# Kernel optimization log

Measured on AMD Instinct MI355X. Metric: run time of the kernel, lower is better.

Reference implementation:

```python
import jax, jax.numpy as jnp
import numpy as np

N_HEADS = 8
D_EMBED = 1024
D_CROSS = 768
D_HEAD = D_EMBED // N_HEADS


def setup_inputs() -> dict:
    key = jax.random.key(0)
    ks = jax.random.split(key, 10)
    B, SQ, SKV = 8, 4096, 77
    scale_e = 1.0 / np.sqrt(D_EMBED)
    scale_c = 1.0 / np.sqrt(D_CROSS)
    return {
        "x": jax.random.normal(ks[0], (B, SQ, D_EMBED), dtype=jnp.float32),
        "y": jax.random.normal(ks[1], (B, SKV, D_CROSS), dtype=jnp.float32),
        # weights stored as [in, out] so projection is x @ W + b
        "Wq": jax.random.normal(ks[2], (D_EMBED, D_EMBED), dtype=jnp.float32) * scale_e,
        "bq": jnp.zeros((D_EMBED,), dtype=jnp.float32),
        "Wk": jax.random.normal(ks[3], (D_CROSS, D_EMBED), dtype=jnp.float32) * scale_c,
        "bk": jnp.zeros((D_EMBED,), dtype=jnp.float32),
        "Wv": jax.random.normal(ks[4], (D_CROSS, D_EMBED), dtype=jnp.float32) * scale_c,
        "bv": jnp.zeros((D_EMBED,), dtype=jnp.float32),
        "Wo": jax.random.normal(ks[5], (D_EMBED, D_EMBED), dtype=jnp.float32) * scale_e,
        "bo": jnp.zeros((D_EMBED,), dtype=jnp.float32),
    }


def reference(x, y, Wq, bq, Wk, bk, Wv, bv, Wo, bo):
    B, SQ, _ = x.shape
    # projections
    q = x @ Wq + bq                      # [B, SQ, D_EMBED]
    k = y @ Wk + bk                      # [B, SKV, D_EMBED]
    v = y @ Wv + bv                      # [B, SKV, D_EMBED]
    # split heads -> [B, H, S, Dh]
    q = q.reshape(B, SQ, N_HEADS, D_HEAD).transpose(0, 2, 1, 3)
    k = k.reshape(B, -1, N_HEADS, D_HEAD).transpose(0, 2, 1, 3)
    v = v.reshape(B, -1, N_HEADS, D_HEAD).transpose(0, 2, 1, 3)
    # attention: q@k^T / sqrt(d_head), softmax, @v
    scale = 1.0 / jnp.sqrt(jnp.asarray(D_HEAD, dtype=q.dtype))
    weight = jnp.einsum("bhqd,bhkd->bhqk", q, k) * scale  # [B, H, SQ, SKV]
    weight = jax.nn.softmax(weight, axis=-1)
    out = jnp.einsum("bhqk,bhkd->bhqd", weight, v)        # [B, H, SQ, Dh]
    out = out.transpose(0, 2, 1, 3).reshape(B, SQ, D_EMBED)
    return out @ Wo + bo
```

## Files before the change

kernel.cpp:

```cpp
#include <hip/hip_runtime.h>

typedef _Float16 half_t;
typedef _Float16 half8 __attribute__((ext_vector_type(8)));
typedef float f32x4 __attribute__((ext_vector_type(4)));

#define D_EMBED   1024
#define D_CROSS   768
#define N_HEADS   8
#define D_HEAD    128
#define BATCH     8
#define SEQ_Q     4096
#define SEQ_KV    77
#define SKV_PAD   80
#define NKV       (N_HEADS*SKV_PAD)
#define M_Q       (BATCH*SEQ_Q)

#define WS_S     ((size_t)0)
#define WS_WQC   (WS_S    + (size_t)M_Q*NKV*2)
#define WS_WOT   (WS_WQC  + (size_t)D_EMBED*D_EMBED*2)
#define WS_WKVT  (WS_WOT  + (size_t)D_EMBED*D_EMBED*2)
#define WS_YH    (WS_WKVT + (size_t)2*D_EMBED*D_CROSS*2)
#define WS_KV    (WS_YH   + (size_t)BATCH*SKV_PAD*D_CROSS*2)
#define WS_BKV   (WS_KV   + (size_t)BATCH*SKV_PAD*2*D_EMBED*2)
#define WS_BT1   (WS_BKV  + (size_t)2*D_EMBED*4)
#define WS_BT2   (WS_BT1  + (size_t)BATCH*NKV*D_EMBED*2)
#define WS_C1    (WS_BT2  + (size_t)BATCH*D_EMBED*NKV*2)

#define ATTN_SCALE 0.08838834764831845f

__device__ __forceinline__ void gload_lds16(const void* g, void* lds) {
  __builtin_amdgcn_global_load_lds(
      (const __attribute__((address_space(1))) unsigned int*)g,
      (__attribute__((address_space(3))) unsigned int*)lds, 16, 0, 0);
}
__device__ __forceinline__ void BAR() {
  __builtin_amdgcn_s_barrier();
  __builtin_amdgcn_sched_barrier(0);
}

__global__ void cast_f32_f16(const float* __restrict__ src, half_t* __restrict__ dst) {
  int i = blockIdx.x * 256 + threadIdx.x;
  f32x4 a = *(const f32x4*)(src + (size_t)i*8);
  f32x4 b = *(const f32x4*)(src + (size_t)i*8 + 4);
  half8 h;
#pragma unroll
  for (int j = 0; j < 4; ++j) { h[j] = (half_t)a[j]; h[j+4] = (half_t)b[j]; }
  *(half8*)(dst + (size_t)i*8) = h;
}

__global__ void transpose_f32f16(const float* __restrict__ src, half_t* __restrict__ dst,
                                 int K, int N) {
  __shared__ float tile[32][33];
  int n0 = blockIdx.x * 32, k0 = blockIdx.y * 32;
  int tx = threadIdx.x, ty = threadIdx.y;
#pragma unroll
  for (int j = 0; j < 4; ++j)
    tile[ty + j*8][tx] = src[(size_t)(k0 + ty + j*8)*N + n0 + tx];
  __syncthreads();
#pragma unroll
  for (int j = 0; j < 4; ++j)
    dst[(size_t)(n0 + ty + j*8)*K + k0 + tx] = (half_t)tile[tx][ty + j*8];
}

__global__ void convert_pad_y(const float* __restrict__ y, half_t* __restrict__ yh) {
  int idx = blockIdx.x * 256 + threadIdx.x;
  int r = idx / D_CROSS, col = idx - r*D_CROSS;
  int b = r / SKV_PAD, s = r - b*SKV_PAD;
  yh[idx] = (s < SEQ_KV) ? (half_t)y[(size_t)(b*SEQ_KV + s)*D_CROSS + col] : (half_t)0.f;
}

__global__ void concat_bias(const float* __restrict__ bk, const float* __restrict__ bv,
                            float* __restrict__ bkv) {
  int i = blockIdx.x * 256 + threadIdx.x;
  bkv[i] = (i < D_EMBED) ? bk[i] : bv[i - D_EMBED];
}

__global__ __launch_bounds__(256, 3)
void gemm_kv(const half_t* __restrict__ A, const half_t* __restrict__ Bt,
             const float* __restrict__ bias, half_t* __restrict__ C,
             int M, int N, int K) {
  __shared__ half_t As[3][128*32];
  __shared__ half_t Bs[2][128*32];
  const int tid = threadIdx.x;
  const int l = tid & 63, w = tid >> 6;
  const int l4 = l & 15, lh = l >> 4;
  const int bn0 = blockIdx.x * 128, bm0 = blockIdx.y * 128;
  const int wr = w >> 1, wc = w & 1;
  const int rslot = lh << 4;
  f32x4 acc[4][4] = {};
  const int nk = K >> 5;
  const int srow = w*16 + (l >> 2);
  const int scol = (l & 3)*8;

  auto stageB = [&](int kt, int bb) {
    const half_t* g = Bt + (size_t)(bn0 + srow)*K + scol + kt*32;
    gload_lds16(g,                 (char*)Bs[bb] + w*1024);
    gload_lds16(g + (size_t)64*K,  (char*)Bs[bb] + 4096 + w*1024);
  };
  auto stageA = [&](int kt, int bb) {
    const half_t* g = A + (size_t)(bm0 + srow)*K + scol + kt*32;
    gload_lds16(g,                 (char*)As[bb] + w*1024);
    gload_lds16(g + (size_t)64*K,  (char*)As[bb] + 4096 + w*1024);
  };
  auto compute = [&](int ab, int bb) {
    half8 af[4], bf[4];
#pragma unroll
    for (int m = 0; m < 4; ++m)
      af[m] = *(const half8*)((const char*)As[ab] + (size_t)(wr*64 + m*16 + l4)*64 + rslot);
#pragma unroll
    for (int n = 0; n < 4; ++n)
      bf[n] = *(const half8*)((const char*)Bs[bb] + (size_t)(wc*64 + n*16 + l4)*64 + rslot);
#pragma unroll
    for (int m = 0; m < 4; ++m)
#pragma unroll
      for (int n = 0; n < 4; ++n)
        acc[m][n] = __builtin_amdgcn_mfma_f32_16x16x32_f16(af[m], bf[n], acc[m][n], 0, 0, 0);
  };

  stageA(0, 0); stageA(1, 1); stageB(0, 0);
  asm volatile("s_waitcnt vmcnt(0)" ::: "memory");
  BAR();
  int aCur = 0, aP2 = 2;
  for (int t = 0; t < nk; ++t) {
    if (t + 1 < nk) stageB(t + 1, (t + 1) & 1);
    if (t + 2 < nk) stageA(t + 2, aP2);
    compute(aCur, t & 1);
    if (t + 1 < nk) {
      if (t + 2 < nk) { asm volatile("s_waitcnt vmcnt(2)" ::: "memory"); }
      else            { asm volatile("s_waitcnt vmcnt(0)" ::: "memory"); }
      BAR();
    }
    aCur = (aCur == 2) ? 0 : aCur + 1;
    aP2  = (aP2  == 2) ? 0 : aP2  + 1;
  }

  const int cb = bn0 + wc*64, rb = bm0 + wr*64;
#pragma unroll
  for (int n = 0; n < 4; ++n) {
    const int col = cb + n*16 + l4;
    const float bvv = bias[col];
#pragma unroll
    for (int m = 0; m < 4; ++m)
#pragma unroll
      for (int j = 0; j < 4; ++j)
        C[(size_t)(rb + m*16 + lh*4 + j)*N + col] = (half_t)(acc[m][n][j] + bvv);
  }
}

__global__ __launch_bounds__(256, 2)
void w1_build(const half_t* __restrict__ kvb, const half_t* __restrict__ Wqc,
              half_t* __restrict__ Bt1) {
  __shared__ half_t K_lds[80*136];
  const int blk = blockIdx.x;
  const int b = blk >> 3, h = blk & 7;
  const int tid = threadIdx.x;
  const int l = tid & 63, w = tid >> 6;
  const int l4 = l & 15, lh = l >> 4;
  for (int i = tid; i < 80*16; i += 256) {
    int s = i >> 4, d = (i & 15) << 3;
    *(half8*)(K_lds + s*136 + d) =
        *(const half8*)(kvb + (size_t)(b*SKV_PAD + s)*2048 + h*128 + d);
  }
  __syncthreads();
  for (int c = 0; c < 4; ++c) {
    f32x4 acc[5][4] = {};
#pragma unroll
    for (int kt = 0; kt < 4; ++kt) {
      half8 af[5], bf[4];
#pragma unroll
      for (int m = 0; m < 5; ++m)
        af[m] = *(const half8*)(K_lds + (size_t)(m*16 + l4)*136 + kt*32 + lh*8);
#pragma unroll
      for (int n = 0; n < 4; ++n)
        bf[n] = *(const half8*)(Wqc + (size_t)(w*256 + c*64 + n*16 + l4)*1024 + h*128 + kt*32 + lh*8);
#pragma unroll
      for (int m = 0; m < 5; ++m)
#pragma unroll
        for (int n = 0; n < 4; ++n)
          acc[m][n] = __builtin_amdgcn_mfma_f32_16x16x32_f16(af[m], bf[n], acc[m][n], 0, 0, 0);
    }
#pragma unroll
    for (int n = 0; n < 4; ++n) {
      const int colk = w*256 + c*64 + n*16 + l4;
#pragma unroll
      for (int m = 0; m < 5; ++m)
#pragma unroll
        for (int j = 0; j < 4; ++j) {
          const int srow = m*16 + lh*4 + j;
          size_t byte = (((size_t)(b*NKV + h*SKV_PAD + srow))*1024 + colk)*2;
          byte ^= ((size_t)((srow >> 1) & 3)) << 4;
          *(half_t*)((char*)Bt1 + byte) = (half_t)(acc[m][n][j]*ATTN_SCALE);
        }
    }
  }
}

__global__ __launch_bounds__(256, 2)
void w2_build(const half_t* __restrict__ kvb, const half_t* __restrict__ Wot,
              half_t* __restrict__ Bt2) {
  __shared__ half_t V_lds[80*136];
  const int blk = blockIdx.x;
  const int b = blk >> 3, h = blk & 7;
  const int tid = threadIdx.x;
  const int l = tid & 63, w = tid >> 6;
  const int l4 = l & 15, lh = l >> 4;
  for (int i = tid; i < 80*16; i += 256) {
    int s = i >> 4, d = (i & 15) << 3;
    *(half8*)(V_lds + s*136 + d) =
        *(const half8*)(kvb + (size_t)(b*SKV_PAD + s)*2048 + 1024 + h*128 + d);
  }
  __syncthreads();
  for (int c = 0; c < 4; ++c) {
    f32x4 acc[4][5] = {};
#pragma unroll
    for (int kt = 0; kt < 4; ++kt) {
      half8 af[4], bf[5];
#pragma unroll
      for (int m = 0; m < 4; ++m)
        af[m] = *(const half8*)(Wot + (size_t)(w*256 + c*64 + m*16 + l4)*1024 + h*128 + kt*32 + lh*8);
#pragma unroll
      for (int n = 0; n < 5; ++n)
        bf[n] = *(const half8*)(V_lds + (size_t)(n*16 + l4)*136 + kt*32 + lh*8);
#pragma unroll
      for (int m = 0; m < 4; ++m)
#pragma unroll
        for (int n = 0; n < 5; ++n)
          acc[m][n] = __builtin_amdgcn_mfma_f32_16x16x32_f16(af[m], bf[n], acc[m][n], 0, 0, 0);
    }
#pragma unroll
    for (int m = 0; m < 4; ++m) {
#pragma unroll
      for (int j = 0; j < 4; ++j) {
        const int nrow = w*256 + c*64 + m*16 + lh*4 + j;
#pragma unroll
        for (int n = 0; n < 5; ++n) {
          const int scol = n*16 + l4;
          size_t byte = (((size_t)(b*1024 + nrow))*NKV + h*SKV_PAD + scol)*2;
          byte ^= ((size_t)((nrow >> 1) & 3)) << 4;
          *(half_t*)((char*)Bt2 + byte) = (half_t)acc[m][n][j];
        }
      }
    }
  }
}

__global__ void c1_build(const half_t* __restrict__ kvb, const float* __restrict__ bq,
                         float* __restrict__ c1) {
  int idx = blockIdx.x * 256 + threadIdx.x;
  int b = idx / NKV, n = idx - b*NKV;
  int h = n / SKV_PAD, s = n - h*SKV_PAD;
  const half_t* kp = kvb + (size_t)(b*SKV_PAD + s)*2048 + h*128;
  float acc = 0.f;
#pragma unroll 8
  for (int d = 0; d < 128; ++d) acc += bq[h*128 + d] * (float)kp[d];
  c1[idx] = acc * ATTN_SCALE;
}

template<bool AF32, bool OUTF32, int NBX>
__global__ __launch_bounds__(256, 3)
void gemm_bt(const void* __restrict__ Av, const half_t* __restrict__ BtAll,
             const float* __restrict__ biasAll, void* __restrict__ Cv,
             int M, int N, int K, int btBatchStride, int biasBatchStride) {
  __shared__ half_t As[AF32 ? 2 : 3][128*32];
  __shared__ half_t Bs[AF32 ? 3 : 2][128*32];
  const int tid = threadIdx.x;
  const int l  = tid & 63;
  const int w  = tid >> 6;
  const int l4 = l & 15, lh = l >> 4;

  const int chunk = (int)gridDim.x >> 3;
  const int sb = blockIdx.x;
  const int lin = (sb & 7)*chunk + (sb >> 3);
  const int bx = lin % NBX;
  const int by = lin / NBX;
  const int b  = by >> 5;
  const half_t* Bt  = BtAll  + (size_t)b*btBatchStride;
  const float* bias = biasAll + (size_t)b*biasBatchStride;

  const int bn0 = bx * 128;
  const int bm0 = by * 128;
  const int wr = w >> 1, wc = w & 1;
  const int aslot = lh << 4;
  const int bslot = (lh ^ ((l4 >> 1) & 3)) << 4;

  f32x4 acc[4][4] = {};
  const int nk = K >> 5;
  const int srow = w*16 + (l >> 2);
  const int scol = (l & 3)*8;

  auto stageB = [&](int kt, int bb) {
    const half_t* g = Bt + (size_t)(bn0 + srow)*K + scol + kt*32;
    gload_lds16(g,                (char*)Bs[bb] + w*1024);
    gload_lds16(g + (size_t)64*K, (char*)Bs[bb] + 4096 + w*1024);
  };
  auto stageA16 = [&](int kt, int bb) {
    const half_t* A = (const half_t*)Av;
    const half_t* g = A + (size_t)(bm0 + srow)*K + scol + kt*32;
    gload_lds16(g,                (char*)As[bb] + w*1024);
    gload_lds16(g + (size_t)64*K, (char*)As[bb] + 4096 + w*1024);
  };

  f32x4 L0, L1, L2, L3;
  const int arow = tid >> 2;
  const int ac0  = (tid & 3) * 8;
  const int wslot = (tid & 3) << 4;
  auto aload = [&](int kt) {
    const float* A = (const float*)Av;
    const float* g0 = A + (size_t)(bm0 + arow)*K + kt*32 + ac0;
    const float* g1 = A + (size_t)(bm0 + 64 + arow)*K + kt*32 + ac0;
    L0 = *(const f32x4*)g0; L1 = *(const f32x4*)(g0 + 4);
    L2 = *(const f32x4*)g1; L3 = *(const f32x4*)(g1 + 4);
  };
  auto awrite = [&](int bb) {
    half8 h0, h1;
#pragma unroll
    for (int j = 0; j < 4; ++j) { h0[j] = (half_t)L0[j]; h0[j+4] = (half_t)L1[j]; }
#pragma unroll
    for (int j = 0; j < 4; ++j) { h1[j] = (half_t)L2[j]; h1[j+4] = (half_t)L3[j]; }
    *(half8*)((char*)As[bb] + (size_t)arow*64 + wslot)        = h0;
    *(half8*)((char*)As[bb] + (size_t)(64 + arow)*64 + wslot) = h1;
  };

  auto compute = [&](int ab, int bb) {
    half8 af[4], bf[4];
#pragma unroll
    for (int m = 0; m < 4; ++m)
      af[m] = *(const half8*)((const char*)As[ab] + (size_t)(wr*64 + m*16 + l4)*64 + aslot);
#pragma unroll
    for (int n = 0; n < 4; ++n)
      bf[n] = *(const half8*)((const char*)Bs[bb] + (size_t)(wc*64 + n*16 + l4)*64 + bslot);
#pragma unroll
    for (int m = 0; m < 4; ++m)
#pragma unroll
      for (int n = 0; n < 4; ++n)
        acc[m][n] = __builtin_amdgcn_mfma_f32_16x16x32_f16(af[m], bf[n], acc[m][n], 0, 0, 0);
  };

  if constexpr (!AF32) {
    stageA16(0, 0); stageA16(1, 1); stageB(0, 0);
    asm volatile("s_waitcnt vmcnt(0)" ::: "memory");
    BAR();
    int aCur = 0, aP2 = 2;
    for (int t = 0; t < nk; ++t) {
      if (t + 1 < nk) stageB(t + 1, (t + 1) & 1);
      if (t + 2 < nk) stageA16(t + 2, aP2);
      compute(aCur, t & 1);
      if (t + 1 < nk) {
        if (t + 2 < nk) { asm volatile("s_waitcnt vmcnt(2)" ::: "memory"); }
        else            { asm volatile("s_waitcnt vmcnt(0)" ::: "memory"); }
        BAR();
      }
      aCur = (aCur == 2) ? 0 : aCur + 1;
      aP2  = (aP2  == 2) ? 0 : aP2  + 1;
    }
  } else {
    aload(0); stageB(0, 0); stageB(1, 1);
    awrite(0);
    asm volatile("s_waitcnt vmcnt(2) lgkmcnt(0)" ::: "memory");
    BAR();
    int bCur = 0, bP2 = 2;
    for (int t = 0; t < nk; ++t) {
      if (t + 1 < nk) aload(t + 1);
      if (t + 2 < nk) stageB(t + 2, bP2);
      compute(t & 1, bCur);
      if (t + 1 < nk) {
        awrite((t + 1) & 1);
        asm volatile("s_waitcnt lgkmcnt(0)" ::: "memory");
        BAR();
      }
      bCur = (bCur == 2) ? 0 : bCur + 1;
      bP2  = (bP2  == 2) ? 0 : bP2  + 1;
    }
  }

  const int c_base = bn0 + wc*64;
  const int r_base = bm0 + wr*64;
#pragma unroll
  for (int n = 0; n < 4; ++n) {
    const int col = c_base + n*16 + l4;
    const float bvv = bias[col];
#pragma unroll
    for (int m = 0; m < 4; ++m) {
#pragma unroll
      for (int j = 0; j < 4; ++j) {
        const int row = r_base + m*16 + lh*4 + j;
        const float v = acc[m][n][j] + bvv;
        if constexpr (OUTF32) ((float*)Cv)[(size_t)row*N + col] = v;
        else                  ((half_t*)Cv)[(size_t)row*N + col] = (half_t)v;
      }
    }
  }
}

__global__ __launch_bounds__(256, 4)
void softmax_inplace(half_t* __restrict__ S) {
  const int gid = blockIdx.x * 256 + threadIdx.x;
  const int row = gid >> 3, h = gid & 7;
  half_t* p = S + (size_t)row*NKV + h*SKV_PAD;
  half8 v[10];
#pragma unroll
  for (int i = 0; i < 10; ++i) v[i] = *(const half8*)(p + i*8);
  float mx = -1e30f;
#pragma unroll
  for (int i = 0; i < 10; ++i)
#pragma unroll
    for (int j = 0; j < 8; ++j) {
      if (i*8 + j < SEQ_KV) mx = fmaxf(mx, (float)v[i][j]);
    }
  float sm = 0.f;
#pragma unroll
  for (int i = 0; i < 10; ++i) {
    half8 t = v[i];
#pragma unroll
    for (int j = 0; j < 8; ++j) {
      float e = (i*8 + j < SEQ_KV) ? __expf((float)t[j] - mx) : 0.f;
      sm += e;
      t[j] = (half_t)e;
    }
    v[i] = t;
  }
  const float inv = 1.f / sm;
#pragma unroll
  for (int i = 0; i < 10; ++i) {
    half8 t = v[i];
#pragma unroll
    for (int j = 0; j < 8; ++j) t[j] = (half_t)((float)t[j] * inv);
    *(half8*)(p + i*8) = t;
  }
}

extern "C" void kernel_launch(void* const* d_in, const int* in_sizes, int n_in,
                              void* d_out, int out_size, void* d_ws, size_t ws_size,
                              hipStream_t stream) {
  (void)in_sizes; (void)n_in; (void)out_size; (void)ws_size;
  const float* x  = (const float*)d_in[0];
  const float* y  = (const float*)d_in[1];
  const float* Wq = (const float*)d_in[2];
  const float* bq = (const float*)d_in[3];
  const float* Wk = (const float*)d_in[4];
  const float* bk = (const float*)d_in[5];
  const float* Wv = (const float*)d_in[6];
  const float* bv = (const float*)d_in[7];
  const float* Wo = (const float*)d_in[8];
  const float* bo = (const float*)d_in[9];

  char* ws = (char*)d_ws;
  half_t* S    = (half_t*)(ws + WS_S);
  half_t* Wqc  = (half_t*)(ws + WS_WQC);
  half_t* Wot  = (half_t*)(ws + WS_WOT);
  half_t* Wkvt = (half_t*)(ws + WS_WKVT);
  half_t* yh   = (half_t*)(ws + WS_YH);
  half_t* kvb  = (half_t*)(ws + WS_KV);
  float*  bkv  = (float*)(ws + WS_BKV);
  half_t* Bt1  = (half_t*)(ws + WS_BT1);
  half_t* Bt2  = (half_t*)(ws + WS_BT2);
  float*  c1   = (float*)(ws + WS_C1);

  dim3 tb(32, 8);
  cast_f32_f16<<<512, 256, 0, stream>>>(Wq, Wqc);
  transpose_f32f16<<<dim3(32, 32), tb, 0, stream>>>(Wo, Wot, 1024, 1024);
  transpose_f32f16<<<dim3(32, 24), tb, 0, stream>>>(Wk, Wkvt, 768, 1024);
  transpose_f32f16<<<dim3(32, 24), tb, 0, stream>>>(Wv, Wkvt + (size_t)1024*768, 768, 1024);
  convert_pad_y<<<BATCH*SKV_PAD*D_CROSS/256, 256, 0, stream>>>(y, yh);
  concat_bias<<<2*D_EMBED/256, 256, 0, stream>>>(bk, bv, bkv);

  gemm_kv<<<dim3(16, 5), 256, 0, stream>>>(yh, Wkvt, bkv, kvb, BATCH*SKV_PAD, 2048, 768);

  c1_build<<<BATCH*NKV/256, 256, 0, stream>>>(kvb, bq, c1);
  w1_build<<<BATCH*N_HEADS, 256, 0, stream>>>(kvb, Wqc, Bt1);
  w2_build<<<BATCH*N_HEADS, 256, 0, stream>>>(kvb, Wot, Bt2);

  gemm_bt<true, false, 5><<<1280, 256, 0, stream>>>(
      x, Bt1, c1, S, M_Q, NKV, 1024, NKV*1024, NKV);

  softmax_inplace<<<M_Q*N_HEADS/256, 256, 0, stream>>>(S);

  gemm_bt<false, true, 8><<<2048, 256, 0, stream>>>(
      S, Bt2, bo, (float*)d_out, M_Q, 1024, NKV, 1024*NKV, 0);
}
```

Measured before the change: 289.5 us.

## Replace output GEMM with 256x256 8-wave pingpong kernel and swizzled S layout

```diff
diff --git a/kernel.cpp b/kernel.cpp
--- a/kernel.cpp
+++ b/kernel.cpp
@@ -232,11 +232,12 @@
 #pragma unroll
       for (int j = 0; j < 4; ++j) {
         const int nrow = w*256 + c*64 + m*16 + lh*4 + j;
+        const size_t rowbase = ((size_t)(b*1024 + nrow))*1280;
 #pragma unroll
         for (int n = 0; n < 5; ++n) {
-          const int scol = n*16 + l4;
-          size_t byte = (((size_t)(b*1024 + nrow))*NKV + h*SKV_PAD + scol)*2;
-          byte ^= ((size_t)((nrow >> 1) & 3)) << 4;
+          const int cc = h*80 + n*16 + l4;
+          size_t byte = rowbase + (size_t)(cc >> 6)*128
+                        + ((size_t)(((cc >> 3) & 7) ^ (nrow & 7)) << 4) + ((cc & 7) << 1);
           *(half_t*)((char*)Bt2 + byte) = (half_t)acc[m][n][j];
         }
       }
@@ -256,13 +257,13 @@
   c1[idx] = acc * ATTN_SCALE;
 }
 
-template<bool AF32, bool OUTF32, int NBX>
+template<int NBX>
 __global__ __launch_bounds__(256, 3)
-void gemm_bt(const void* __restrict__ Av, const half_t* __restrict__ BtAll,
-             const float* __restrict__ biasAll, void* __restrict__ Cv,
-             int M, int N, int K, int btBatchStride, int biasBatchStride) {
-  __shared__ half_t As[AF32 ? 2 : 3][128*32];
-  __shared__ half_t Bs[AF32 ? 3 : 2][128*32];
+void gemm_s(const float* __restrict__ Av, const half_t* __restrict__ BtAll,
+            const float* __restrict__ biasAll, half_t* __restrict__ Cv,
+            int M, int N, int K) {
+  __shared__ half_t As[2][128*32];
+  __shared__ half_t Bs[3][128*32];
   const int tid = threadIdx.x;
   const int l  = tid & 63;
   const int w  = tid >> 6;
@@ -274,8 +275,8 @@
   const int bx = lin % NBX;
   const int by = lin / NBX;
   const int b  = by >> 5;
-  const half_t* Bt  = BtAll  + (size_t)b*btBatchStride;
-  const float* bias = biasAll + (size_t)b*biasBatchStride;
+  const half_t* Bt  = BtAll  + (size_t)b*NKV*1024;
+  const float* bias = biasAll + (size_t)b*NKV;
 
   const int bn0 = bx * 128;
   const int bm0 = by * 128;
@@ -293,21 +294,14 @@
     gload_lds16(g,                (char*)Bs[bb] + w*1024);
     gload_lds16(g + (size_t)64*K, (char*)Bs[bb] + 4096 + w*1024);
   };
-  auto stageA16 = [&](int kt, int bb) {
-    const half_t* A = (const half_t*)Av;
-    const half_t* g = A + (size_t)(bm0 + srow)*K + scol + kt*32;
-    gload_lds16(g,                (char*)As[bb] + w*1024);
-    gload_lds16(g + (size_t)64*K, (char*)As[bb] + 4096 + w*1024);
-  };
 
   f32x4 L0, L1, L2, L3;
   const int arow = tid >> 2;
   const int ac0  = (tid & 3) * 8;
   const int wslot = (tid & 3) << 4;
   auto aload = [&](int kt) {
-    const float* A = (const float*)Av;
-    const float* g0 = A + (size_t)(bm0 + arow)*K + kt*32 + ac0;
-    const float* g1 = A + (size_t)(bm0 + 64 + arow)*K + kt*32 + ac0;
+    const float* g0 = Av + (size_t)(bm0 + arow)*K + kt*32 + ac0;
+    const float* g1 = Av + (size_t)(bm0 + 64 + arow)*K + kt*32 + ac0;
     L0 = *(const f32x4*)g0; L1 = *(const f32x4*)(g0 + 4);
     L2 = *(const f32x4*)g1; L3 = *(const f32x4*)(g1 + 4);
   };
@@ -336,41 +330,22 @@
         acc[m][n] = __builtin_amdgcn_mfma_f32_16x16x32_f16(af[m], bf[n], acc[m][n], 0, 0, 0);
   };
 
-  if constexpr (!AF32) {
-    stageA16(0, 0); stageA16(1, 1); stageB(0, 0);
-    asm volatile("s_waitcnt vmcnt(0)" ::: "memory");
-    BAR();
-    int aCur = 0, aP2 = 2;
-    for (int t = 0; t < nk; ++t) {
-      if (t + 1 < nk) stageB(t + 1, (t + 1) & 1);
-      if (t + 2 < nk) stageA16(t + 2, aP2);
-      compute(aCur, t & 1);
-      if (t + 1 < nk) {
-        if (t + 2 < nk) { asm volatile("s_waitcnt vmcnt(2)" ::: "memory"); }
-        else            { asm volatile("s_waitcnt vmcnt(0)" ::: "memory"); }
-        BAR();
-      }
-      aCur = (aCur == 2) ? 0 : aCur + 1;
-      aP2  = (aP2  == 2) ? 0 : aP2  + 1;
-    }
-  } else {
-    aload(0); stageB(0, 0); stageB(1, 1);
-    awrite(0);
-    asm volatile("s_waitcnt vmcnt(2) lgkmcnt(0)" ::: "memory");
-    BAR();
-    int bCur = 0, bP2 = 2;
-    for (int t = 0; t < nk; ++t) {
-      if (t + 1 < nk) aload(t + 1);
-      if (t + 2 < nk) stageB(t + 2, bP2);
-      compute(t & 1, bCur);
-      if (t + 1 < nk) {
-        awrite((t + 1) & 1);
-        asm volatile("s_waitcnt lgkmcnt(0)" ::: "memory");
-        BAR();
-      }
-      bCur = (bCur == 2) ? 0 : bCur + 1;
-      bP2  = (bP2  == 2) ? 0 : bP2  + 1;
-    }
+  aload(0); stageB(0, 0); stageB(1, 1);
+  awrite(0);
+  asm volatile("s_waitcnt vmcnt(2) lgkmcnt(0)" ::: "memory");
+  BAR();
+  int bCur = 0, bP2 = 2;
+  for (int t = 0; t < nk; ++t) {
+    if (t + 1 < nk) aload(t + 1);
+    if (t + 2 < nk) stageB(t + 2, bP2);
+    compute(t & 1, bCur);
+    if (t + 1 < nk) {
+      awrite((t + 1) & 1);
+      asm volatile("s_waitcnt lgkmcnt(0)" ::: "memory");
+      BAR();
+    }
+    bCur = (bCur == 2) ? 0 : bCur + 1;
+    bP2  = (bP2  == 2) ? 0 : bP2  + 1;
   }
 
   const int c_base = bn0 + wc*64;
@@ -385,8 +360,9 @@
       for (int j = 0; j < 4; ++j) {
         const int row = r_base + m*16 + lh*4 + j;
         const float v = acc[m][n][j] + bvv;
-        if constexpr (OUTF32) ((float*)Cv)[(size_t)row*N + col] = v;
-        else                  ((half_t*)Cv)[(size_t)row*N + col] = (half_t)v;
+        size_t byte = (size_t)row*1280 + (size_t)(col >> 6)*128
+                      + ((size_t)(((col >> 3) & 7) ^ (row & 7)) << 4) + ((col & 7) << 1);
+        *(half_t*)((char*)Cv + byte) = (half_t)v;
       }
     }
   }
@@ -396,17 +372,22 @@
 void softmax_inplace(half_t* __restrict__ S) {
   const int gid = blockIdx.x * 256 + threadIdx.x;
   const int row = gid >> 3, h = gid & 7;
-  half_t* p = S + (size_t)row*NKV + h*SKV_PAD;
+  const int key = row & 7;
+  char* base = (char*)S + (size_t)row*1280;
+  size_t off[10];
   half8 v[10];
 #pragma unroll
-  for (int i = 0; i < 10; ++i) v[i] = *(const half8*)(p + i*8);
+  for (int i = 0; i < 10; ++i) {
+    const int ls = h*10 + i;
+    off[i] = (size_t)(ls >> 3)*128 + ((size_t)((ls & 7) ^ key) << 4);
+    v[i] = *(const half8*)(base + off[i]);
+  }
   float mx = -1e30f;
 #pragma unroll
   for (int i = 0; i < 10; ++i)
 #pragma unroll
-    for (int j = 0; j < 8; ++j) {
+    for (int j = 0; j < 8; ++j)
       if (i*8 + j < SEQ_KV) mx = fmaxf(mx, (float)v[i][j]);
-    }
   float sm = 0.f;
 #pragma unroll
   for (int i = 0; i < 10; ++i) {
@@ -414,8 +395,7 @@
 #pragma unroll
     for (int j = 0; j < 8; ++j) {
       float e = (i*8 + j < SEQ_KV) ? __expf((float)t[j] - mx) : 0.f;
-      sm += e;
-      t[j] = (half_t)e;
+      sm += e; t[j] = (half_t)e;
     }
     v[i] = t;
   }
@@ -425,7 +405,121 @@
     half8 t = v[i];
 #pragma unroll
     for (int j = 0; j < 8; ++j) t[j] = (half_t)((float)t[j] * inv);
-    *(half8*)(p + i*8) = t;
+    *(half8*)(base + off[i]) = t;
+  }
+}
+
+#define PH8(Q, ABASE, PRE, TAIL)                                                                     \
+  {                                                                                                  \
+    half8 a00 = *(const half8*)((ABASE) + (size_t)(arow0 + (2*(Q)  )*16)*128 + ak0);                 \
+    half8 a01 = *(const half8*)((ABASE) + (size_t)(arow0 + (2*(Q)  )*16)*128 + ak1);                 \
+    half8 a10 = *(const half8*)((ABASE) + (size_t)(arow0 + (2*(Q)+1)*16)*128 + ak0);                 \
+    half8 a11 = *(const half8*)((ABASE) + (size_t)(arow0 + (2*(Q)+1)*16)*128 + ak1);                 \
+    PRE;                                                                                             \
+    __builtin_amdgcn_s_barrier();                                                                    \
+    asm volatile("s_waitcnt lgkmcnt(0)" ::: "memory");                                               \
+    __builtin_amdgcn_sched_barrier(0);                                                               \
+    __builtin_amdgcn_s_setprio(1);                                                                   \
+    _Pragma("unroll")                                                                                \
+    for (int ni = 0; ni < 4; ++ni) {                                                                 \
+      acc[2*(Q)  ][ni] = __builtin_amdgcn_mfma_f32_16x16x32_f16(a00, bf[ni][0], acc[2*(Q)  ][ni],0,0,0); \
+      acc[2*(Q)  ][ni] = __builtin_amdgcn_mfma_f32_16x16x32_f16(a01, bf[ni][1], acc[2*(Q)  ][ni],0,0,0); \
+      acc[2*(Q)+1][ni] = __builtin_amdgcn_mfma_f32_16x16x32_f16(a10, bf[ni][0], acc[2*(Q)+1][ni],0,0,0); \
+      acc[2*(Q)+1][ni] = __builtin_amdgcn_mfma_f32_16x16x32_f16(a11, bf[ni][1], acc[2*(Q)+1][ni],0,0,0); \
+    }                                                                                                \
+    __builtin_amdgcn_s_setprio(0);                                                                   \
+    TAIL;                                                                                            \
+    __builtin_amdgcn_s_barrier();                                                                    \
+    __builtin_amdgcn_sched_barrier(0);                                                               \
+  }
+
+__global__ __launch_bounds__(512, 1)
+void gemm8p_out(const half_t* __restrict__ Sa, const half_t* __restrict__ Bt2,
+                const float* __restrict__ bo, float* __restrict__ out) {
+  __shared__ half_t AbS[2*256*64];
+  __shared__ half_t BbS[2*256*64];
+  char* ABp = (char*)AbS;
+  char* BBp = (char*)BbS;
+  const int tid = threadIdx.x;
+  const int l = tid & 63, w = tid >> 6;
+  const int l4 = l & 15, lh = l >> 4;
+  const int lin = ((int)blockIdx.x & 7)*64 + ((int)blockIdx.x >> 3);
+  const int bx = lin & 3, by = lin >> 2;
+  const int bm0 = by << 8, bn0 = bx << 8;
+  const half_t* Bt = Bt2 + (size_t)(by >> 4)*1024*640;
+  const int wr = w >> 2, wc = w & 3;
+  const int ak0 = ((lh    ) ^ (l4 & 7)) << 4;
+  const int ak1 = ((lh + 4) ^ (l4 & 7)) << 4;
+  const int arow0 = wr*128 + l4;
+  const int brow0 = wc*64 + l4;
+  f32x4 acc[8][4] = {};
+  half8 bf[4][2];
+
+  auto stA = [&](int kt, int db, int hf) {
+#pragma unroll
+    for (int r = 0; r < 2; ++r) {
+      const int id = tid + r*512;
+      gload_lds16((const char*)Sa + (size_t)(bm0 + hf*128 + (id >> 3))*1280 + (size_t)kt*128 + (id & 7)*16,
+                  ABp + db*32768 + hf*16384 + r*8192 + w*1024);
+    }
+  };
+  auto stB = [&](int kt, int db, int hf) {
+#pragma unroll
+    for (int r = 0; r < 2; ++r) {
+      const int id = tid + r*512;
+      gload_lds16((const char*)Bt + (size_t)(bn0 + hf*128 + (id >> 3))*1280 + (size_t)kt*128 + (id & 7)*16,
+                  BBp + db*32768 + hf*16384 + r*8192 + w*1024);
+    }
+  };
+  auto rdB = [&](const char* base) {
+#pragma unroll
+    for (int ni = 0; ni < 4; ++ni) {
+      bf[ni][0] = *(const half8*)(base + (size_t)(brow0 + ni*16)*128 + ak0);
+      bf[ni][1] = *(const half8*)(base + (size_t)(brow0 + ni*16)*128 + ak1);
+    }
+  };
+
+  stA(0, 0, 0); stA(0, 0, 1); stB(0, 0, 0); stB(0, 0, 1); stB(1, 1, 0); stB(1, 1, 1);
+  asm volatile("s_waitcnt vmcnt(4)" ::: "memory");
+  __builtin_amdgcn_sched_barrier(0);
+  __builtin_amdgcn_s_barrier();
+
+  const char* A0 = ABp;            const char* A1 = ABp + 32768;
+  const char* B0 = BBp;            const char* B1 = BBp + 32768;
+
+  for (int u = 0; u < 5; ++u) {
+    const int kt0 = 2*u, kt1 = 2*u + 1;
+    const bool nx = (u < 4);
+    PH8(0, A0, { rdB(B0); stA(kt1, 1, 0); stA(kt1, 1, 1); }, {});
+    PH8(1, A0, { if (nx) stB(kt0 + 2, 0, 0); }, {});
+    PH8(2, A0, { if (nx) stB(kt0 + 2, 0, 1); }, {});
+    PH8(3, A0, {}, {
+      if (nx) { asm volatile("s_waitcnt vmcnt(4)" ::: "memory"); }
+      else    { asm volatile("s_waitcnt vmcnt(0)" ::: "memory"); }
+      __builtin_amdgcn_sched_barrier(0);
+    });
+    PH8(0, A1, { rdB(B1); if (nx) stA(kt0 + 2, 0, 0); }, {});
+    PH8(1, A1, { if (nx) stA(kt0 + 2, 0, 1); }, {});
+    PH8(2, A1, { if (nx) stB(kt1 + 2, 1, 0); }, {});
+    PH8(3, A1, { if (nx) stB(kt1 + 2, 1, 1); }, {
+      if (nx) {
+        asm volatile("s_waitcnt vmcnt(4)" ::: "memory");
+        __builtin_amdgcn_sched_barrier(0);
+      }
+    });
+  }
+
+#pragma unroll
+  for (int ni = 0; ni < 4; ++ni) {
+    const int col = bn0 + wc*64 + ni*16 + l4;
+    const float bvv = bo[col];
+#pragma unroll
+    for (int mi = 0; mi < 8; ++mi)
+#pragma unroll
+      for (int j = 0; j < 4; ++j) {
+        const int row = bm0 + wr*128 + mi*16 + lh*4 + j;
+        out[(size_t)row*1024 + col] = acc[mi][ni][j] + bvv;
+      }
   }
 }
 
@@ -470,11 +564,9 @@
   w1_build<<<BATCH*N_HEADS, 256, 0, stream>>>(kvb, Wqc, Bt1);
   w2_build<<<BATCH*N_HEADS, 256, 0, stream>>>(kvb, Wot, Bt2);
 
-  gemm_bt<true, false, 5><<<1280, 256, 0, stream>>>(
-      x, Bt1, c1, S, M_Q, NKV, 1024, NKV*1024, NKV);
+  gemm_s<5><<<1280, 256, 0, stream>>>(x, Bt1, c1, S, M_Q, NKV, 1024);
 
   softmax_inplace<<<M_Q*N_HEADS/256, 256, 0, stream>>>(S);
 
-  gemm_bt<false, true, 8><<<2048, 256, 0, stream>>>(
-      S, Bt2, bo, (float*)d_out, M_Q, 1024, NKV, 1024*NKV, 0);
-}
+  gemm8p_out<<<512, 512, 0, stream>>>(S, Bt2, bo, (float*)d_out);
+}
```

Measured after the change: 290.9 us. Within noise of the previous version (+0.5%).

## Fuse score GEMM, softmax and output GEMM into one kernel

Applied to the files above, without the earlier changes.

```diff
diff --git a/kernel.cpp b/kernel.cpp
--- a/kernel.cpp
+++ b/kernel.cpp
@@ -13,6 +13,7 @@
 #define SEQ_KV    77
 #define SKV_PAD   80
 #define NKV       (N_HEADS*SKV_PAD)
+#define NKV_PAD   768
 #define M_Q       (BATCH*SEQ_Q)
 
 #define WS_S     ((size_t)0)
@@ -23,7 +24,7 @@
 #define WS_KV    (WS_YH   + (size_t)BATCH*SKV_PAD*D_CROSS*2)
 #define WS_BKV   (WS_KV   + (size_t)BATCH*SKV_PAD*2*D_EMBED*2)
 #define WS_BT1   (WS_BKV  + (size_t)2*D_EMBED*4)
-#define WS_BT2   (WS_BT1  + (size_t)BATCH*NKV*D_EMBED*2)
+#define WS_BT2   (WS_BT1  + (size_t)BATCH*NKV_PAD*D_EMBED*2)
 #define WS_C1    (WS_BT2  + (size_t)BATCH*D_EMBED*NKV*2)
 
 #define ATTN_SCALE 0.08838834764831845f
@@ -186,9 +187,9 @@
       for (int m = 0; m < 5; ++m)
 #pragma unroll
         for (int j = 0; j < 4; ++j) {
-          const int srow = m*16 + lh*4 + j;
-          size_t byte = (((size_t)(b*NKV + h*SKV_PAD + srow))*1024 + colk)*2;
-          byte ^= ((size_t)((srow >> 1) & 3)) << 4;
+          const int r = h*SKV_PAD + m*16 + lh*4 + j;
+          size_t byte = ((size_t)(b*NKV_PAD + r))*2048 + (size_t)(colk >> 6)*128
+                        + ((size_t)(((colk >> 3) & 7) ^ (r & 7)) << 4) + ((colk & 7) << 1);
           *(half_t*)((char*)Bt1 + byte) = (half_t)(acc[m][n][j]*ATTN_SCALE);
         }
     }
@@ -232,11 +233,12 @@
 #pragma unroll
       for (int j = 0; j < 4; ++j) {
         const int nrow = w*256 + c*64 + m*16 + lh*4 + j;
+        const size_t rowbase = ((size_t)(b*1024 + nrow))*1280;
 #pragma unroll
         for (int n = 0; n < 5; ++n) {
-          const int scol = n*16 + l4;
-          size_t byte = (((size_t)(b*1024 + nrow))*NKV + h*SKV_PAD + scol)*2;
-          byte ^= ((size_t)((nrow >> 1) & 3)) << 4;
+          const int cc = h*80 + n*16 + l4;
+          size_t byte = rowbase + (size_t)(cc >> 6)*128
+                        + ((size_t)(((cc >> 3) & 7) ^ (nrow & 7)) << 4) + ((cc & 7) << 1);
           *(half_t*)((char*)Bt2 + byte) = (half_t)acc[m][n][j];
         }
       }
@@ -256,176 +258,151 @@
   c1[idx] = acc * ATTN_SCALE;
 }
 
-template<bool AF32, bool OUTF32, int NBX>
-__global__ __launch_bounds__(256, 3)
-void gemm_bt(const void* __restrict__ Av, const half_t* __restrict__ BtAll,
-             const float* __restrict__ biasAll, void* __restrict__ Cv,
-             int M, int N, int K, int btBatchStride, int biasBatchStride) {
-  __shared__ half_t As[AF32 ? 2 : 3][128*32];
-  __shared__ half_t Bs[AF32 ? 3 : 2][128*32];
+__global__ __launch_bounds__(512, 2)
+void fused_sv(const float* __restrict__ X, const half_t* __restrict__ Bt1,
+              const float* __restrict__ c1, const half_t* __restrict__ Bt2,
+              const float* __restrict__ bo, float* __restrict__ out) {
+  __shared__ half_t S_lds[64*640];
+  __shared__ half_t x_lds[2][64*64];
   const int tid = threadIdx.x;
-  const int l  = tid & 63;
-  const int w  = tid >> 6;
+  const int l = tid & 63, w = tid >> 6;
   const int l4 = l & 15, lh = l >> 4;
-
-  const int chunk = (int)gridDim.x >> 3;
-  const int sb = blockIdx.x;
-  const int lin = (sb & 7)*chunk + (sb >> 3);
-  const int bx = lin % NBX;
-  const int by = lin / NBX;
-  const int b  = by >> 5;
-  const half_t* Bt  = BtAll  + (size_t)b*btBatchStride;
-  const float* bias = biasAll + (size_t)b*biasBatchStride;
-
-  const int bn0 = bx * 128;
-  const int bm0 = by * 128;
-  const int wr = w >> 1, wc = w & 1;
-  const int aslot = lh << 4;
-  const int bslot = (lh ^ ((l4 >> 1) & 3)) << 4;
-
-  f32x4 acc[4][4] = {};
-  const int nk = K >> 5;
-  const int srow = w*16 + (l >> 2);
-  const int scol = (l & 3)*8;
-
-  auto stageB = [&](int kt, int bb) {
-    const half_t* g = Bt + (size_t)(bn0 + srow)*K + scol + kt*32;
-    gload_lds16(g,                (char*)Bs[bb] + w*1024);
-    gload_lds16(g + (size_t)64*K, (char*)Bs[bb] + 4096 + w*1024);
+  const int k7 = l4 & 7;
+
+  const int lin = ((int)blockIdx.x & 7)*64 + ((int)blockIdx.x >> 3);
+  const int batch = lin >> 6;
+  const int row0 = batch*SEQ_Q + (lin & 63)*64;
+  const half_t* W1 = Bt1 + (size_t)batch*NKV_PAD*1024;
+  const half_t* W2 = Bt2 + (size_t)batch*1024*NKV;
+  const float* c1b = c1 + batch*NKV;
+
+  f32x4 sacc[4][5] = {};
+  const int nfb = w*5;
+
+  const int xrow = tid >> 3, xc8 = tid & 7;
+  const float* xg = X + (size_t)(row0 + xrow)*1024 + xc8*8;
+  f32x4 xa, xb;
+  auto xload = [&](int kc) {
+    const float* g = xg + kc*64;
+    xa = *(const f32x4*)g; xb = *(const f32x4*)(g + 4);
   };
-  auto stageA16 = [&](int kt, int bb) {
-    const half_t* A = (const half_t*)Av;
-    const half_t* g = A + (size_t)(bm0 + srow)*K + scol + kt*32;
-    gload_lds16(g,                (char*)As[bb] + w*1024);
-    gload_lds16(g + (size_t)64*K, (char*)As[bb] + 4096 + w*1024);
+  auto xwrite = [&](int buf) {
+    half8 h;
+#pragma unroll
+    for (int e = 0; e < 4; ++e) { h[e] = (half_t)xa[e]; h[e+4] = (half_t)xb[e]; }
+    *(half8*)((char*)x_lds[buf] + xrow*128 + ((xc8 ^ (xrow & 7)) << 4)) = h;
   };
 
-  f32x4 L0, L1, L2, L3;
-  const int arow = tid >> 2;
-  const int ac0  = (tid & 3) * 8;
-  const int wslot = (tid & 3) << 4;
-  auto aload = [&](int kt) {
-    const float* A = (const float*)Av;
-    const float* g0 = A + (size_t)(bm0 + arow)*K + kt*32 + ac0;
-    const float* g1 = A + (size_t)(bm0 + 64 + arow)*K + kt*32 + ac0;
-    L0 = *(const f32x4*)g0; L1 = *(const f32x4*)(g0 + 4);
-    L2 = *(const f32x4*)g1; L3 = *(const f32x4*)(g1 + 4);
-  };
-  auto awrite = [&](int bb) {
-    half8 h0, h1;
-#pragma unroll
-    for (int j = 0; j < 4; ++j) { h0[j] = (half_t)L0[j]; h0[j+4] = (half_t)L1[j]; }
-#pragma unroll
-    for (int j = 0; j < 4; ++j) { h1[j] = (half_t)L2[j]; h1[j+4] = (half_t)L3[j]; }
-    *(half8*)((char*)As[bb] + (size_t)arow*64 + wslot)        = h0;
-    *(half8*)((char*)As[bb] + (size_t)(64 + arow)*64 + wslot) = h1;
-  };
-
-  auto compute = [&](int ab, int bb) {
-    half8 af[4], bf[4];
-#pragma unroll
-    for (int m = 0; m < 4; ++m)
-      af[m] = *(const half8*)((const char*)As[ab] + (size_t)(wr*64 + m*16 + l4)*64 + aslot);
-#pragma unroll
-    for (int n = 0; n < 4; ++n)
-      bf[n] = *(const half8*)((const char*)Bs[bb] + (size_t)(wc*64 + n*16 + l4)*64 + bslot);
-#pragma unroll
-    for (int m = 0; m < 4; ++m)
-#pragma unroll
-      for (int n = 0; n < 4; ++n)
-        acc[m][n] = __builtin_amdgcn_mfma_f32_16x16x32_f16(af[m], bf[n], acc[m][n], 0, 0, 0);
-  };
-
-  if constexpr (!AF32) {
-    stageA16(0, 0); stageA16(1, 1); stageB(0, 0);
-    asm volatile("s_waitcnt vmcnt(0)" ::: "memory");
-    BAR();
-    int aCur = 0, aP2 = 2;
-    for (int t = 0; t < nk; ++t) {
-      if (t + 1 < nk) stageB(t + 1, (t + 1) & 1);
-      if (t + 2 < nk) stageA16(t + 2, aP2);
-      compute(aCur, t & 1);
-      if (t + 1 < nk) {
-        if (t + 2 < nk) { asm volatile("s_waitcnt vmcnt(2)" ::: "memory"); }
-        else            { asm volatile("s_waitcnt vmcnt(0)" ::: "memory"); }
-        BAR();
+  xload(0); xwrite(0);
+  __syncthreads();
+
+  for (int kc = 0; kc < 16; ++kc) {
+    if (kc + 1 < 16) xload(kc + 1);
+    const char* xc = (const char*)x_lds[kc & 1];
+#pragma unroll
+    for (int kk = 0; kk < 2; ++kk) {
+      half8 af[4];
+#pragma unroll
+      for (int m = 0; m < 4; ++m)
+        af[m] = *(const half8*)(xc + (size_t)(m*16 + l4)*128 + (((kk*4 + lh) ^ k7) << 4));
+#pragma unroll
+      for (int nf = 0; nf < 5; ++nf) {
+        const int nrow = (nfb + nf)*16 + l4;
+        half8 bfv = *(const half8*)((const char*)W1 + (size_t)nrow*2048 + (size_t)kc*128
+                                    + (((kk*4 + lh) ^ k7) << 4));
+#pragma unroll
+        for (int m = 0; m < 4; ++m)
+          sacc[m][nf] = __builtin_amdgcn_mfma_f32_16x16x32_f16(af[m], bfv, sacc[m][nf], 0, 0, 0);
       }
-      aCur = (aCur == 2) ? 0 : aCur + 1;
-      aP2  = (aP2  == 2) ? 0 : aP2  + 1;
-    }
-  } else {
-    aload(0); stageB(0, 0); stageB(1, 1);
-    awrite(0);
-    asm volatile("s_waitcnt vmcnt(2) lgkmcnt(0)" ::: "memory");
-    BAR();
-    int bCur = 0, bP2 = 2;
-    for (int t = 0; t < nk; ++t) {
-      if (t + 1 < nk) aload(t + 1);
-      if (t + 2 < nk) stageB(t + 2, bP2);
-      compute(t & 1, bCur);
-      if (t + 1 < nk) {
-        awrite((t + 1) & 1);
-        asm volatile("s_waitcnt lgkmcnt(0)" ::: "memory");
-        BAR();
+    }
+    if (kc + 1 < 16) {
+      xwrite((kc + 1) & 1);
+      __syncthreads();
+    }
+  }
+
+#pragma unroll
+  for (int nf = 0; nf < 5; ++nf) {
+    const int col = (nfb + nf)*16 + l4;
+#pragma unroll
+    for (int m = 0; m < 4; ++m)
+#pragma unroll
+      for (int j = 0; j < 4; ++j) {
+        const int row = m*16 + lh*4 + j;
+        size_t byte = (size_t)row*1280 + (size_t)(col >> 6)*128
+                      + ((size_t)(((col >> 3) & 7) ^ (row & 7)) << 4) + ((col & 7) << 1);
+        *(half_t*)((char*)S_lds + byte) = (half_t)sacc[m][nf][j];
       }
-      bCur = (bCur == 2) ? 0 : bCur + 1;
-      bP2  = (bP2  == 2) ? 0 : bP2  + 1;
-    }
-  }
-
-  const int c_base = bn0 + wc*64;
-  const int r_base = bm0 + wr*64;
-#pragma unroll
-  for (int n = 0; n < 4; ++n) {
-    const int col = c_base + n*16 + l4;
-    const float bvv = bias[col];
-#pragma unroll
-    for (int m = 0; m < 4; ++m) {
+  }
+  __syncthreads();
+
+  {
+    const int row = tid >> 3, h = tid & 7;
+    const int key = row & 7;
+    char* base = (char*)S_lds + (size_t)row*1280;
+    float fv[10][8];
+    float mx = -1e30f;
+#pragma unroll
+    for (int i = 0; i < 10; ++i) {
+      const int ls = h*10 + i;
+      half8 v = *(const half8*)(base + (size_t)(ls >> 3)*128 + ((size_t)((ls & 7) ^ key) << 4));
+      f32x4 ca = *(const f32x4*)(c1b + h*80 + i*8);
+      f32x4 cb = *(const f32x4*)(c1b + h*80 + i*8 + 4);
+#pragma unroll
+      for (int j = 0; j < 8; ++j) {
+        const float cc = (j < 4) ? ca[j] : cb[j - 4];
+        const float sv = (float)v[j] + cc;
+        const bool ok = (i*8 + j) < SEQ_KV;
+        fv[i][j] = ok ? sv : -1e30f;
+        if (ok) mx = fmaxf(mx, sv);
+      }
+    }
+    float sm = 0.f;
+#pragma unroll
+    for (int i = 0; i < 10; ++i)
+#pragma unroll
+      for (int j = 0; j < 8; ++j) { float e = __expf(fv[i][j] - mx); sm += e; fv[i][j] = e; }
+    const float inv = 1.f / sm;
+#pragma unroll
+    for (int i = 0; i < 10; ++i) {
+      const int ls = h*10 + i;
+      half8 t;
+#pragma unroll
+      for (int j = 0; j < 8; ++j) t[j] = (half_t)(fv[i][j] * inv);
+      *(half8*)(base + (size_t)(ls >> 3)*128 + ((size_t)((ls & 7) ^ key) << 4)) = t;
+    }
+  }
+  __syncthreads();
+
+  f32x4 oacc[4][8] = {};
+  const int ncb = w*128;
+  for (int ks = 0; ks < 20; ++ks) {
+    const size_t koff = (size_t)(ks >> 1)*128 + ((((ks & 1)*4 + lh) ^ k7) << 4);
+    half8 af[4];
+#pragma unroll
+    for (int m = 0; m < 4; ++m)
+      af[m] = *(const half8*)((const char*)S_lds + (size_t)(m*16 + l4)*1280 + koff);
+#pragma unroll
+    for (int nf = 0; nf < 8; ++nf) {
+      const int nrow = ncb + nf*16 + l4;
+      half8 bfv = *(const half8*)((const char*)W2 + (size_t)nrow*1280 + koff);
+#pragma unroll
+      for (int m = 0; m < 4; ++m)
+        oacc[m][nf] = __builtin_amdgcn_mfma_f32_16x16x32_f16(af[m], bfv, oacc[m][nf], 0, 0, 0);
+    }
+  }
+
+#pragma unroll
+  for (int nf = 0; nf < 8; ++nf) {
+    const int col = ncb + nf*16 + l4;
+    const float bvv = bo[col];
+#pragma unroll
+    for (int m = 0; m < 4; ++m)
 #pragma unroll
       for (int j = 0; j < 4; ++j) {
-        const int row = r_base + m*16 + lh*4 + j;
-        const float v = acc[m][n][j] + bvv;
-        if constexpr (OUTF32) ((float*)Cv)[(size_t)row*N + col] = v;
-        else                  ((half_t*)Cv)[(size_t)row*N + col] = (half_t)v;
+        const int row = row0 + m*16 + lh*4 + j;
+        out[(size_t)row*1024 + col] = oacc[m][nf][j] + bvv;
       }
-    }
-  }
-}
-
-__global__ __launch_bounds__(256, 4)
-void softmax_inplace(half_t* __restrict__ S) {
-  const int gid = blockIdx.x * 256 + threadIdx.x;
-  const int row = gid >> 3, h = gid & 7;
-  half_t* p = S + (size_t)row*NKV + h*SKV_PAD;
-  half8 v[10];
-#pragma unroll
-  for (int i = 0; i < 10; ++i) v[i] = *(const half8*)(p + i*8);
-  float mx = -1e30f;
-#pragma unroll
-  for (int i = 0; i < 10; ++i)
-#pragma unroll
-    for (int j = 0; j < 8; ++j) {
-      if (i*8 + j < SEQ_KV) mx = fmaxf(mx, (float)v[i][j]);
-    }
-  float sm = 0.f;
-#pragma unroll
-  for (int i = 0; i < 10; ++i) {
-    half8 t = v[i];
-#pragma unroll
-    for (int j = 0; j < 8; ++j) {
-      float e = (i*8 + j < SEQ_KV) ? __expf((float)t[j] - mx) : 0.f;
-      sm += e;
-      t[j] = (half_t)e;
-    }
-    v[i] = t;
-  }
-  const float inv = 1.f / sm;
-#pragma unroll
-  for (int i = 0; i < 10; ++i) {
-    half8 t = v[i];
-#pragma unroll
-    for (int j = 0; j < 8; ++j) t[j] = (half_t)((float)t[j] * inv);
-    *(half8*)(p + i*8) = t;
   }
 }
 
@@ -445,7 +422,6 @@
   const float* bo = (const float*)d_in[9];
 
   char* ws = (char*)d_ws;
-  half_t* S    = (half_t*)(ws + WS_S);
   half_t* Wqc  = (half_t*)(ws + WS_WQC);
   half_t* Wot  = (half_t*)(ws + WS_WOT);
   half_t* Wkvt = (half_t*)(ws + WS_WKVT);
@@ -470,11 +446,5 @@
   w1_build<<<BATCH*N_HEADS, 256, 0, stream>>>(kvb, Wqc, Bt1);
   w2_build<<<BATCH*N_HEADS, 256, 0, stream>>>(kvb, Wot, Bt2);
 
-  gemm_bt<true, false, 5><<<1280, 256, 0, stream>>>(
-      x, Bt1, c1, S, M_Q, NKV, 1024, NKV*1024, NKV);
-
-  softmax_inplace<<<M_Q*N_HEADS/256, 256, 0, stream>>>(S);
-
-  gemm_bt<false, true, 8><<<2048, 256, 0, stream>>>(
-      S, Bt2, bo, (float*)d_out, M_Q, 1024, NKV, 1024*NKV, 0);
-}
+  fused_sv<<<512, 512, 0, stream>>>(x, Bt1, c1, Bt2, bo, (float*)d_out);
+}
```

Result: faster. 259.3 us (median of 2 runs) (-10.4%).
